# Performance work log

Measured on AMD Instinct MI355X. Metric: run time of the kernel, lower is better.

The kernel has to match this reference:

```python
import jax, jax.numpy as jnp
import numpy as np

B, T, C = 8, 2048, 640

def setup_inputs() -> dict:
    key = jax.random.key(0)
    k1, k2, k3, k4 = jax.random.split(key, 4)
    s = 1.0 / np.sqrt(C)  # ~ torch Linear default init scale
    x = jax.random.normal(k1, (B, T, C), dtype=jnp.float32)
    w_q = jax.random.normal(k2, (C, C), dtype=jnp.float32) * s
    w_k = jax.random.normal(k3, (C, C), dtype=jnp.float32) * s
    w_v = jax.random.normal(k4, (C, C), dtype=jnp.float32) * s
    return {"x": x, "w_q": w_q, "w_k": w_k, "w_v": w_v}

def reference(x, w_q, w_k, w_v):
    # nn.Linear computes x @ W.T; weights here stored as (out, in) like torch.
    q = jnp.einsum('btc,oc->bto', x, w_q)
    k = jnp.einsum('btc,oc->bto', x, w_k)
    v = jnp.einsum('btc,oc->bto', x, w_v)
    scale = jnp.sqrt(jnp.asarray(C, dtype=x.dtype))  # note: full n_embd, not per-head
    scores = jnp.einsum('bqc,bkc->bqk', q, k) / scale  # [B,T,T]
    Tn = x.shape[1]
    causal = jnp.triu(jnp.ones((Tn, Tn), dtype=bool), k=1)
    scores = jnp.where(causal[None, :, :], jnp.asarray(-jnp.inf, dtype=x.dtype), scores)
    attn = jax.nn.softmax(scores, axis=-1)
    attn_out = jnp.einsum('bqk,bkc->bqc', attn, v)
    return x + attn_out
```

## Files before the change

kernel.cpp:

```cpp
#include <hip/hip_runtime.h>
#include <stdint.h>
#include <stddef.h>

#define T_SEQ 2048
#define C_DIM 640
#define N_BATCH 8

typedef __bf16 bf16x8 __attribute__((ext_vector_type(8)));
typedef float f32x4 __attribute__((ext_vector_type(4)));

__device__ __forceinline__ unsigned short f2bf(float f) {
  unsigned u = __float_as_uint(f);
  u += 0x7fffu + ((u >> 16) & 1u);
  return (unsigned short)(u >> 16);
}
__device__ __forceinline__ float bf2f(unsigned short h) {
  return __uint_as_float(((unsigned)h) << 16);
}

__device__ __forceinline__ void gll16(const unsigned short* src, unsigned short* dst) {
  __builtin_amdgcn_global_load_lds(
      (const __attribute__((address_space(1))) void*)src,
      (__attribute__((address_space(3))) void*)dst, 16, 0, 0);
}

__device__ __forceinline__ void stage_tile(const unsigned short* gbase, int ldg,
                                           unsigned short* lbuf, int wave, int lane) {
#pragma unroll
  for (int i = 0; i < 4; ++i) {
    const int o   = i * 4096 + wave * 1024 + lane * 16;
    const int row = o >> 7;
    const int cb  = o & 127;
    const int scb = cb ^ ((row & 7) << 4);
    const unsigned short* src = gbase + (size_t)row * ldg + (scb >> 1);
    unsigned short* dst = lbuf + ((i * 4096 + wave * 1024) >> 1);
    gll16(src, dst);
  }
}

__device__ __forceinline__ void tri_decode(int t, int& mi, int& ni) {
  int m = (int)((__fsqrt_rn(8.0f * (float)t + 1.0f) - 1.0f) * 0.5f);
  while ((m + 1) * (m + 2) / 2 <= t) ++m;
  while (m * (m + 1) / 2 > t) --m;
  mi = m;
  ni = t - m * (m + 1) / 2;
}

template <int MODE>
__global__ __launch_bounds__(256) void gemm_k(
    const unsigned short* __restrict__ Abase, const unsigned short* __restrict__ Bbase,
    const unsigned short* __restrict__ B2base, unsigned short* __restrict__ OutB,
    unsigned short* __restrict__ OutB2, float* __restrict__ OutF,
    const float* __restrict__ Lrow, const unsigned short* __restrict__ Xres,
    float* __restrict__ Lpart) {
  const int lin = blockIdx.x;
  int mi, ni, bz;
  if constexpr (MODE == 0) {
    const int wg = (lin & 7) * 160 + (lin >> 3);
    mi = wg / 10;
    const int t = wg % 10;
    bz = t / 5;
    ni = t % 5;
  } else if constexpr (MODE == 1) {
    const int wg = (lin & 7) * 136 + (lin >> 3);
    bz = wg / 136;
    tri_decode(wg % 136, mi, ni);
  } else if constexpr (MODE == 2) {
    const int wg = (lin & 7) * 80 + (lin >> 3);
    bz = wg / 80;
    const int t = wg % 80;
    mi = 15 - t / 5;
    ni = t % 5;
  } else {
    bz = lin / 25;
    const int rem = lin % 25;
    mi = rem / 5;
    ni = rem % 5;
  }

  __shared__ unsigned short As[2][8192];
  __shared__ unsigned short Bs[2][8192];
  const int tid = threadIdx.x;
  const int wave = tid >> 6, lane = tid & 63;
  const int wm = wave >> 1, wn = wave & 1;

  const unsigned short* Ap;
  const unsigned short* Bp;
  int ldA, ldB, ksteps;
  if constexpr (MODE == 0) {
    Ap = Abase + (size_t)mi * 81920;
    Bp = ((bz == 0) ? Bbase : B2base) + (size_t)ni * 81920;
    ldA = 640; ldB = 640; ksteps = 10;
  } else if constexpr (MODE == 1) {
    Ap = Abase + (size_t)bz * 1310720 + (size_t)mi * 81920;
    Bp = Bbase + (size_t)bz * 1310720 + (size_t)ni * 81920;
    ldA = 640; ldB = 640; ksteps = 10;
  } else if constexpr (MODE == 2) {
    Ap = Abase + (size_t)bz * 4194304 + (size_t)mi * 262144;
    Bp = Bbase + (size_t)bz * 1310720 + (size_t)ni * 262144;
    ldA = 2048; ldB = 2048; ksteps = 2 * (mi + 1);
  } else {
    Ap = Abase + (size_t)mi * 81920 + bz * 128;
    Bp = Bbase + (size_t)ni * 81920 + bz * 128;
    ldA = 640; ldB = 640; ksteps = 2;
  }

  f32x4 acc[4][4] = {};

  stage_tile(Ap, ldA, As[0], wave, lane);
  stage_tile(Bp, ldB, Bs[0], wave, lane);
  __syncthreads();

  int cur = 0;
  for (int t = 0; t < ksteps; ++t) {
    if (t + 1 < ksteps) {
      stage_tile(Ap + (size_t)(t + 1) * 64, ldA, As[cur ^ 1], wave, lane);
      stage_tile(Bp + (size_t)(t + 1) * 64, ldB, Bs[cur ^ 1], wave, lane);
    }
#pragma unroll
    for (int kk = 0; kk < 2; ++kk) {
      bf16x8 af[4], bfr[4];
#pragma unroll
      for (int mt = 0; mt < 4; ++mt) {
        const int row = wm * 64 + mt * 16 + (lane & 15);
        const int cb  = kk * 64 + ((lane >> 4) << 4);
        af[mt] = *(const bf16x8*)&As[cur][row * 64 + ((cb ^ ((row & 7) << 4)) >> 1)];
      }
#pragma unroll
      for (int nt = 0; nt < 4; ++nt) {
        const int row = wn * 64 + nt * 16 + (lane & 15);
        const int cb  = kk * 64 + ((lane >> 4) << 4);
        bfr[nt] = *(const bf16x8*)&Bs[cur][row * 64 + ((cb ^ ((row & 7) << 4)) >> 1)];
      }
#pragma unroll
      for (int mt = 0; mt < 4; ++mt)
#pragma unroll
        for (int nt = 0; nt < 4; ++nt)
          acc[mt][nt] = __builtin_amdgcn_mfma_f32_16x16x32_bf16(af[mt], bfr[nt],
                                                                acc[mt][nt], 0, 0, 0);
    }
    __syncthreads();
    cur ^= 1;
  }

  if constexpr (MODE == 1) {
#pragma unroll
    for (int mt = 0; mt < 4; ++mt) {
      const int r0 = wm * 64 + mt * 16 + ((lane >> 4) << 2);
      const int grow = mi * 128 + r0;
      float rsum[4] = {0.f, 0.f, 0.f, 0.f};
#pragma unroll
      for (int nt = 0; nt < 4; ++nt) {
        const int gc = ni * 128 + wn * 64 + nt * 16 + (lane & 15);
        const size_t base = (size_t)bz * 4194304 + (size_t)grow * 2048 + gc;
#pragma unroll
        for (int r = 0; r < 4; ++r) {
          const float e = (gc <= grow + r) ? __expf(acc[mt][nt][r]) : 0.0f;
          OutB[base + (size_t)r * 2048] = f2bf(e);
          rsum[r] += e;
        }
      }
#pragma unroll
      for (int off = 1; off < 16; off <<= 1) {
#pragma unroll
        for (int r = 0; r < 4; ++r) rsum[r] += __shfl_xor(rsum[r], off);
      }
      if ((lane & 15) == 0) {
#pragma unroll
        for (int r = 0; r < 4; ++r)
          Lpart[((size_t)bz * 2048 + grow + r) * 32 + ni * 2 + wn] = rsum[r];
      }
    }
  } else {
#pragma unroll
    for (int mt = 0; mt < 4; ++mt) {
#pragma unroll
      for (int nt = 0; nt < 4; ++nt) {
        const int r0 = wm * 64 + mt * 16 + ((lane >> 4) << 2);
        const int c  = wn * 64 + nt * 16 + (lane & 15);
        if constexpr (MODE == 0) {
          if (bz == 0) {
            const size_t base = (size_t)(mi * 128 + r0) * 640 + ni * 128 + c;
#pragma unroll
            for (int r = 0; r < 4; ++r) OutB[base + (size_t)r * 640] = f2bf(acc[mt][nt][r]);
          } else {
            const int b = mi >> 4;
            const int tloc = ((mi & 15) << 7) + r0;
            const int gc = ni * 128 + c;
            ushort4 o4;
            o4.x = f2bf(acc[mt][nt][0]); o4.y = f2bf(acc[mt][nt][1]);
            o4.z = f2bf(acc[mt][nt][2]); o4.w = f2bf(acc[mt][nt][3]);
            *(ushort4*)&OutB2[(size_t)b * 1310720 + (size_t)gc * 2048 + tloc] = o4;
          }
        } else if constexpr (MODE == 2) {
          const int grow = mi * 128 + r0;
          const size_t base = (size_t)bz * 1310720 + (size_t)grow * 640 + ni * 128 + c;
#pragma unroll
          for (int r = 0; r < 4; ++r) {
            const float l = Lrow[(size_t)bz * 2048 + grow + r];
            OutF[base + (size_t)r * 640] =
                acc[mt][nt][r] / l + bf2f(Xres[base + (size_t)r * 640]);
          }
        } else {
          const size_t base = (size_t)bz * 409600 + (size_t)(mi * 128 + r0) * 640 + ni * 128 + c;
#pragma unroll
          for (int r = 0; r < 4; ++r) OutF[base + (size_t)r * 640] = acc[mt][nt][r];
        }
      }
    }
  }
}

__global__ void cast_x_k(const float* __restrict__ x, unsigned short* __restrict__ xb, int n4) {
  const int stride = gridDim.x * blockDim.x;
  for (int i = blockIdx.x * blockDim.x + threadIdx.x; i < n4; i += stride) {
    const float4 v = ((const float4*)x)[i];
    ushort4 o;
    o.x = f2bf(v.x); o.y = f2bf(v.y); o.z = f2bf(v.z); o.w = f2bf(v.w);
    ((ushort4*)xb)[i] = o;
  }
}

__global__ void tcast_w(const float* __restrict__ wq, const float* __restrict__ wk,
                        const float* __restrict__ wv, unsigned short* __restrict__ wqT,
                        unsigned short* __restrict__ wkT, unsigned short* __restrict__ wvb) {
  const int z = blockIdx.y;
  const int tx = threadIdx.x, ty = threadIdx.y;
  if (z == 2) {
    const int e = (blockIdx.x * 256 + ty * 32 + tx) * 4;
    const float4 v = *(const float4*)&wv[e];
    ushort4 o;
    o.x = f2bf(v.x); o.y = f2bf(v.y); o.z = f2bf(v.z); o.w = f2bf(v.w);
    *(ushort4*)&wvb[e] = o;
    return;
  }
  __shared__ float tile[32][33];
  const float* w = (z == 0) ? wq : wk;
  unsigned short* wT = (z == 0) ? wqT : wkT;
  const float s = (z == 0) ? 0.03952847075210474f : 1.0f;
  const int bo = (blockIdx.x / 20) * 32, bc = (blockIdx.x % 20) * 32;
#pragma unroll
  for (int i = 0; i < 4; ++i)
    tile[ty + i * 8][tx] = w[(size_t)(bo + ty + i * 8) * 640 + bc + tx];
  __syncthreads();
#pragma unroll
  for (int i = 0; i < 4; ++i)
    wT[(size_t)(bc + ty + i * 8) * 640 + bo + tx] = f2bf(tile[tx][ty + i * 8] * s);
}

__global__ void reduce_mt(const float* __restrict__ Mpart, unsigned short* __restrict__ Mt) {
  const int e = (blockIdx.x * 256 + threadIdx.x) * 4;
  float4 a = *(const float4*)&Mpart[e];
#pragma unroll
  for (int p = 1; p < 5; ++p) {
    const float4 b = *(const float4*)&Mpart[(size_t)p * 409600 + e];
    a.x += b.x; a.y += b.y; a.z += b.z; a.w += b.w;
  }
  ushort4 o;
  o.x = f2bf(a.x); o.y = f2bf(a.y); o.z = f2bf(a.z); o.w = f2bf(a.w);
  *(ushort4*)&Mt[e] = o;
}

__global__ void rowsum_k(const float* __restrict__ Lpart, float* __restrict__ Lr) {
  const int i = blockIdx.x * 256 + threadIdx.x;
  const int jmax = (((i & 2047) >> 7) + 1) * 2;
  const float* p = Lpart + (size_t)i * 32;
  float s = 0.f;
  for (int j = 0; j < jmax; ++j) s += p[j];
  Lr[i] = s;
}

extern "C" void kernel_launch(void* const* d_in, const int* in_sizes, int n_in,
                              void* d_out, int out_size, void* d_ws, size_t ws_size,
                              hipStream_t stream) {
  (void)in_sizes; (void)n_in; (void)out_size; (void)ws_size;
  const float* x  = (const float*)d_in[0];
  const float* wq = (const float*)d_in[1];
  const float* wk = (const float*)d_in[2];
  const float* wv = (const float*)d_in[3];
  float* out = (float*)d_out;

  char* ws = (char*)d_ws;
  unsigned short* xb  = (unsigned short*)(ws + 0);
  unsigned short* wqT = (unsigned short*)(ws + 20971520);
  unsigned short* wkT = (unsigned short*)(ws + 21790720);
  unsigned short* wvb = (unsigned short*)(ws + 22609920);
  unsigned short* Mt  = (unsigned short*)(ws + 23429120);
  unsigned short* y   = (unsigned short*)(ws + 24248320);
  unsigned short* Vt  = (unsigned short*)(ws + 45219840);
  float*          Mpart = (float*)(ws + 66191360);
  float*          Lpart = (float*)(ws + 74383360);
  float*          Lr  = (float*)(ws + 76480512);
  unsigned short* Sb  = (unsigned short*)(ws + 76546048);

  cast_x_k<<<2048, 256, 0, stream>>>(x, xb, 2621440);
  tcast_w<<<dim3(400, 3), dim3(32, 8), 0, stream>>>(wq, wk, wv, wqT, wkT, wvb);
  gemm_k<3><<<125, 256, 0, stream>>>(wkT, wqT, nullptr, nullptr, nullptr, Mpart,
                                     nullptr, nullptr, nullptr);
  reduce_mt<<<400, 256, 0, stream>>>(Mpart, Mt);
  gemm_k<0><<<1280, 256, 0, stream>>>(xb, Mt, wvb, y, Vt, nullptr, nullptr, nullptr,
                                      nullptr);
  gemm_k<1><<<1088, 256, 0, stream>>>(y, xb, nullptr, Sb, nullptr, nullptr, nullptr,
                                      nullptr, Lpart);
  rowsum_k<<<64, 256, 0, stream>>>(Lpart, Lr);
  gemm_k<2><<<640, 256, 0, stream>>>(Sb, Vt, nullptr, nullptr, nullptr, out, Lr, xb,
                                     nullptr);
}
```

Baseline: 152.9 us.

## Fuse score and PV GEMMs into persistent kernel with dependency counters

Replaces the separate score GEMM, row-sum kernel and PV GEMM with one persistent kernel. Workgroups pull work units from an atomic queue ordered by row block, largest first. PV tiles spin-wait on per-(batch,row-block) completion counters and compute the softmax row sums inline. The aim is to remove two kernel launches, the tail idle time between phases, and the separate Lr buffer, at the cost of spin-wait stalls, atomic traffic and possible deadlock if the queue ordering were ever violated.

After: 497.6 us. +225.3%, slower.

```diff
diff --git a/kernel.cpp b/kernel.cpp
--- a/kernel.cpp
+++ b/kernel.cpp
@@ -38,21 +38,11 @@
   }
 }
 
-__device__ __forceinline__ void tri_decode(int t, int& mi, int& ni) {
-  int m = (int)((__fsqrt_rn(8.0f * (float)t + 1.0f) - 1.0f) * 0.5f);
-  while ((m + 1) * (m + 2) / 2 <= t) ++m;
-  while (m * (m + 1) / 2 > t) --m;
-  mi = m;
-  ni = t - m * (m + 1) / 2;
-}
-
 template <int MODE>
 __global__ __launch_bounds__(256) void gemm_k(
     const unsigned short* __restrict__ Abase, const unsigned short* __restrict__ Bbase,
     const unsigned short* __restrict__ B2base, unsigned short* __restrict__ OutB,
-    unsigned short* __restrict__ OutB2, float* __restrict__ OutF,
-    const float* __restrict__ Lrow, const unsigned short* __restrict__ Xres,
-    float* __restrict__ Lpart) {
+    unsigned short* __restrict__ OutB2, float* __restrict__ OutF) {
   const int lin = blockIdx.x;
   int mi, ni, bz;
   if constexpr (MODE == 0) {
@@ -61,16 +51,6 @@
     const int t = wg % 10;
     bz = t / 5;
     ni = t % 5;
-  } else if constexpr (MODE == 1) {
-    const int wg = (lin & 7) * 136 + (lin >> 3);
-    bz = wg / 136;
-    tri_decode(wg % 136, mi, ni);
-  } else if constexpr (MODE == 2) {
-    const int wg = (lin & 7) * 80 + (lin >> 3);
-    bz = wg / 80;
-    const int t = wg % 80;
-    mi = 15 - t / 5;
-    ni = t % 5;
   } else {
     bz = lin / 25;
     const int rem = lin % 25;
@@ -86,36 +66,27 @@
 
   const unsigned short* Ap;
   const unsigned short* Bp;
-  int ldA, ldB, ksteps;
+  int ksteps;
   if constexpr (MODE == 0) {
     Ap = Abase + (size_t)mi * 81920;
     Bp = ((bz == 0) ? Bbase : B2base) + (size_t)ni * 81920;
-    ldA = 640; ldB = 640; ksteps = 10;
-  } else if constexpr (MODE == 1) {
-    Ap = Abase + (size_t)bz * 1310720 + (size_t)mi * 81920;
-    Bp = Bbase + (size_t)bz * 1310720 + (size_t)ni * 81920;
-    ldA = 640; ldB = 640; ksteps = 10;
-  } else if constexpr (MODE == 2) {
-    Ap = Abase + (size_t)bz * 4194304 + (size_t)mi * 262144;
-    Bp = Bbase + (size_t)bz * 1310720 + (size_t)ni * 262144;
-    ldA = 2048; ldB = 2048; ksteps = 2 * (mi + 1);
+    ksteps = 10;
   } else {
     Ap = Abase + (size_t)mi * 81920 + bz * 128;
     Bp = Bbase + (size_t)ni * 81920 + bz * 128;
-    ldA = 640; ldB = 640; ksteps = 2;
+    ksteps = 2;
   }
 
   f32x4 acc[4][4] = {};
-
-  stage_tile(Ap, ldA, As[0], wave, lane);
-  stage_tile(Bp, ldB, Bs[0], wave, lane);
+  stage_tile(Ap, 640, As[0], wave, lane);
+  stage_tile(Bp, 640, Bs[0], wave, lane);
   __syncthreads();
 
   int cur = 0;
   for (int t = 0; t < ksteps; ++t) {
     if (t + 1 < ksteps) {
-      stage_tile(Ap + (size_t)(t + 1) * 64, ldA, As[cur ^ 1], wave, lane);
-      stage_tile(Bp + (size_t)(t + 1) * 64, ldB, Bs[cur ^ 1], wave, lane);
+      stage_tile(Ap + (size_t)(t + 1) * 64, 640, As[cur ^ 1], wave, lane);
+      stage_tile(Bp + (size_t)(t + 1) * 64, 640, Bs[cur ^ 1], wave, lane);
     }
 #pragma unroll
     for (int kk = 0; kk < 2; ++kk) {
@@ -143,68 +114,176 @@
     cur ^= 1;
   }
 
-  if constexpr (MODE == 1) {
-#pragma unroll
-    for (int mt = 0; mt < 4; ++mt) {
+#pragma unroll
+  for (int mt = 0; mt < 4; ++mt) {
+#pragma unroll
+    for (int nt = 0; nt < 4; ++nt) {
       const int r0 = wm * 64 + mt * 16 + ((lane >> 4) << 2);
-      const int grow = mi * 128 + r0;
-      float rsum[4] = {0.f, 0.f, 0.f, 0.f};
-#pragma unroll
-      for (int nt = 0; nt < 4; ++nt) {
-        const int gc = ni * 128 + wn * 64 + nt * 16 + (lane & 15);
-        const size_t base = (size_t)bz * 4194304 + (size_t)grow * 2048 + gc;
-#pragma unroll
-        for (int r = 0; r < 4; ++r) {
-          const float e = (gc <= grow + r) ? __expf(acc[mt][nt][r]) : 0.0f;
-          OutB[base + (size_t)r * 2048] = f2bf(e);
-          rsum[r] += e;
-        }
-      }
-#pragma unroll
-      for (int off = 1; off < 16; off <<= 1) {
-#pragma unroll
-        for (int r = 0; r < 4; ++r) rsum[r] += __shfl_xor(rsum[r], off);
-      }
-      if ((lane & 15) == 0) {
-#pragma unroll
-        for (int r = 0; r < 4; ++r)
-          Lpart[((size_t)bz * 2048 + grow + r) * 32 + ni * 2 + wn] = rsum[r];
-      }
-    }
-  } else {
-#pragma unroll
-    for (int mt = 0; mt < 4; ++mt) {
-#pragma unroll
-      for (int nt = 0; nt < 4; ++nt) {
+      const int c  = wn * 64 + nt * 16 + (lane & 15);
+      if constexpr (MODE == 0) {
+        if (bz == 0) {
+          const size_t base = (size_t)(mi * 128 + r0) * 640 + ni * 128 + c;
+#pragma unroll
+          for (int r = 0; r < 4; ++r) OutB[base + (size_t)r * 640] = f2bf(acc[mt][nt][r]);
+        } else {
+          const int b = mi >> 4;
+          const int tloc = ((mi & 15) << 7) + r0;
+          const int gc = ni * 128 + c;
+          ushort4 o4;
+          o4.x = f2bf(acc[mt][nt][0]); o4.y = f2bf(acc[mt][nt][1]);
+          o4.z = f2bf(acc[mt][nt][2]); o4.w = f2bf(acc[mt][nt][3]);
+          *(ushort4*)&OutB2[(size_t)b * 1310720 + (size_t)gc * 2048 + tloc] = o4;
+        }
+      } else {
+        const size_t base = (size_t)bz * 409600 + (size_t)(mi * 128 + r0) * 640 + ni * 128 + c;
+#pragma unroll
+        for (int r = 0; r < 4; ++r) OutF[base + (size_t)r * 640] = acc[mt][nt][r];
+      }
+    }
+  }
+}
+
+#define NU 1728
+__global__ __launch_bounds__(256) void attn_k(
+    const unsigned short* __restrict__ y, const unsigned short* __restrict__ xb,
+    const unsigned short* __restrict__ Vt, unsigned short* __restrict__ P,
+    float* __restrict__ Lpart, float* __restrict__ out,
+    int* __restrict__ qctr, int* __restrict__ done) {
+  __shared__ unsigned short As[2][8192];
+  __shared__ unsigned short Bs[2][8192];
+  __shared__ float Ls[128];
+  __shared__ int s_u;
+  const int tid = threadIdx.x;
+  const int wave = tid >> 6, lane = tid & 63;
+  const int wm = wave >> 1, wn = wave & 1;
+
+  for (;;) {
+    __syncthreads();
+    if (tid == 0) s_u = atomicAdd(qctr, 1);
+    __syncthreads();
+    const int u = s_u;
+    if (u >= NU) break;
+
+    int rem = u, mi = 0, sub = 0;
+    bool isPV = false;
+    for (int m = 15; m >= 0; --m) {
+      const int a = 8 * (m + 1);
+      if (rem < a) { mi = m; sub = rem; isPV = false; break; }
+      rem -= a;
+      if (rem < 40) { mi = m; sub = rem; isPV = true; break; }
+      rem -= 40;
+    }
+
+    const unsigned short *Ap, *Bp;
+    int ldA, ldB, ksteps, b, nc;
+    if (!isPV) {
+      b = sub / (mi + 1); nc = sub % (mi + 1);
+      Ap = y  + (size_t)b * 1310720 + (size_t)mi * 81920;
+      Bp = xb + (size_t)b * 1310720 + (size_t)nc * 81920;
+      ldA = 640; ldB = 640; ksteps = 10;
+    } else {
+      b = sub / 5; nc = sub % 5;
+      if (tid == 0) {
+        while (__hip_atomic_load(&done[b * 16 + mi], __ATOMIC_ACQUIRE,
+                                 __HIP_MEMORY_SCOPE_AGENT) < mi + 1)
+          __builtin_amdgcn_s_sleep(1);
+      }
+      __syncthreads();
+      if (tid < 128) {
+        const float* p = &Lpart[((size_t)b * 2048 + mi * 128 + tid) * 32];
+        float s = 0.f;
+        const int jm = 2 * (mi + 1);
+        for (int j = 0; j < jm; ++j) s += p[j];
+        Ls[tid] = 1.0f / s;
+      }
+      Ap = P  + (size_t)b * 4194304 + (size_t)mi * 262144;
+      Bp = Vt + (size_t)b * 1310720 + (size_t)nc * 262144;
+      ldA = 2048; ldB = 2048; ksteps = 2 * (mi + 1);
+    }
+
+    f32x4 acc[4][4] = {};
+    stage_tile(Ap, ldA, As[0], wave, lane);
+    stage_tile(Bp, ldB, Bs[0], wave, lane);
+    __syncthreads();
+
+    int cur = 0;
+    for (int t = 0; t < ksteps; ++t) {
+      if (t + 1 < ksteps) {
+        stage_tile(Ap + (size_t)(t + 1) * 64, ldA, As[cur ^ 1], wave, lane);
+        stage_tile(Bp + (size_t)(t + 1) * 64, ldB, Bs[cur ^ 1], wave, lane);
+      }
+#pragma unroll
+      for (int kk = 0; kk < 2; ++kk) {
+        bf16x8 af[4], bfr[4];
+#pragma unroll
+        for (int mt = 0; mt < 4; ++mt) {
+          const int row = wm * 64 + mt * 16 + (lane & 15);
+          const int cb  = kk * 64 + ((lane >> 4) << 4);
+          af[mt] = *(const bf16x8*)&As[cur][row * 64 + ((cb ^ ((row & 7) << 4)) >> 1)];
+        }
+#pragma unroll
+        for (int nt = 0; nt < 4; ++nt) {
+          const int row = wn * 64 + nt * 16 + (lane & 15);
+          const int cb  = kk * 64 + ((lane >> 4) << 4);
+          bfr[nt] = *(const bf16x8*)&Bs[cur][row * 64 + ((cb ^ ((row & 7) << 4)) >> 1)];
+        }
+#pragma unroll
+        for (int mt = 0; mt < 4; ++mt)
+#pragma unroll
+          for (int nt = 0; nt < 4; ++nt)
+            acc[mt][nt] = __builtin_amdgcn_mfma_f32_16x16x32_bf16(af[mt], bfr[nt],
+                                                                  acc[mt][nt], 0, 0, 0);
+      }
+      __syncthreads();
+      cur ^= 1;
+    }
+
+    if (!isPV) {
+#pragma unroll
+      for (int mt = 0; mt < 4; ++mt) {
         const int r0 = wm * 64 + mt * 16 + ((lane >> 4) << 2);
-        const int c  = wn * 64 + nt * 16 + (lane & 15);
-        if constexpr (MODE == 0) {
-          if (bz == 0) {
-            const size_t base = (size_t)(mi * 128 + r0) * 640 + ni * 128 + c;
-#pragma unroll
-            for (int r = 0; r < 4; ++r) OutB[base + (size_t)r * 640] = f2bf(acc[mt][nt][r]);
-          } else {
-            const int b = mi >> 4;
-            const int tloc = ((mi & 15) << 7) + r0;
-            const int gc = ni * 128 + c;
-            ushort4 o4;
-            o4.x = f2bf(acc[mt][nt][0]); o4.y = f2bf(acc[mt][nt][1]);
-            o4.z = f2bf(acc[mt][nt][2]); o4.w = f2bf(acc[mt][nt][3]);
-            *(ushort4*)&OutB2[(size_t)b * 1310720 + (size_t)gc * 2048 + tloc] = o4;
+        const int grow = mi * 128 + r0;
+        float rsum[4] = {0.f, 0.f, 0.f, 0.f};
+#pragma unroll
+        for (int nt = 0; nt < 4; ++nt) {
+          const int gc = nc * 128 + wn * 64 + nt * 16 + (lane & 15);
+          const size_t base = (size_t)b * 4194304 + (size_t)grow * 2048 + gc;
+#pragma unroll
+          for (int r = 0; r < 4; ++r) {
+            const float e = (gc <= grow + r) ? __expf(acc[mt][nt][r]) : 0.0f;
+            P[base + (size_t)r * 2048] = f2bf(e);
+            rsum[r] += e;
           }
-        } else if constexpr (MODE == 2) {
+        }
+#pragma unroll
+        for (int off = 1; off < 16; off <<= 1) {
+#pragma unroll
+          for (int r = 0; r < 4; ++r) rsum[r] += __shfl_xor(rsum[r], off);
+        }
+        if ((lane & 15) == 0) {
+#pragma unroll
+          for (int r = 0; r < 4; ++r)
+            Lpart[((size_t)b * 2048 + grow + r) * 32 + nc * 2 + wn] = rsum[r];
+        }
+      }
+      __threadfence();
+      __syncthreads();
+      if (tid == 0) atomicAdd(&done[b * 16 + mi], 1);
+    } else {
+#pragma unroll
+      for (int mt = 0; mt < 4; ++mt) {
+#pragma unroll
+        for (int nt = 0; nt < 4; ++nt) {
+          const int r0 = wm * 64 + mt * 16 + ((lane >> 4) << 2);
+          const int c  = wn * 64 + nt * 16 + (lane & 15);
           const int grow = mi * 128 + r0;
-          const size_t base = (size_t)bz * 1310720 + (size_t)grow * 640 + ni * 128 + c;
+          const size_t base = (size_t)b * 1310720 + (size_t)grow * 640 + nc * 128 + c;
 #pragma unroll
           for (int r = 0; r < 4; ++r) {
-            const float l = Lrow[(size_t)bz * 2048 + grow + r];
-            OutF[base + (size_t)r * 640] =
-                acc[mt][nt][r] / l + bf2f(Xres[base + (size_t)r * 640]);
+            const float rl = Ls[r0 + r];
+            out[base + (size_t)r * 640] =
+                acc[mt][nt][r] * rl + bf2f(xb[base + (size_t)r * 640]);
           }
-        } else {
-          const size_t base = (size_t)bz * 409600 + (size_t)(mi * 128 + r0) * 640 + ni * 128 + c;
-#pragma unroll
-          for (int r = 0; r < 4; ++r) OutF[base + (size_t)r * 640] = acc[mt][nt][r];
         }
       }
     }
@@ -261,15 +340,6 @@
   *(ushort4*)&Mt[e] = o;
 }
 
-__global__ void rowsum_k(const float* __restrict__ Lpart, float* __restrict__ Lr) {
-  const int i = blockIdx.x * 256 + threadIdx.x;
-  const int jmax = (((i & 2047) >> 7) + 1) * 2;
-  const float* p = Lpart + (size_t)i * 32;
-  float s = 0.f;
-  for (int j = 0; j < jmax; ++j) s += p[j];
-  Lr[i] = s;
-}
-
 extern "C" void kernel_launch(void* const* d_in, const int* in_sizes, int n_in,
                               void* d_out, int out_size, void* d_ws, size_t ws_size,
                               hipStream_t stream) {
@@ -290,19 +360,14 @@
   unsigned short* Vt  = (unsigned short*)(ws + 45219840);
   float*          Mpart = (float*)(ws + 66191360);
   float*          Lpart = (float*)(ws + 74383360);
-  float*          Lr  = (float*)(ws + 76480512);
   unsigned short* Sb  = (unsigned short*)(ws + 76546048);
-
+  int*            ctrs = (int*)(ws + 143654912);
+
+  hipMemsetAsync(ctrs, 0, 1024, stream);
   cast_x_k<<<2048, 256, 0, stream>>>(x, xb, 2621440);
   tcast_w<<<dim3(400, 3), dim3(32, 8), 0, stream>>>(wq, wk, wv, wqT, wkT, wvb);
-  gemm_k<3><<<125, 256, 0, stream>>>(wkT, wqT, nullptr, nullptr, nullptr, Mpart,
-                                     nullptr, nullptr, nullptr);
+  gemm_k<3><<<125, 256, 0, stream>>>(wkT, wqT, nullptr, nullptr, nullptr, Mpart);
   reduce_mt<<<400, 256, 0, stream>>>(Mpart, Mt);
-  gemm_k<0><<<1280, 256, 0, stream>>>(xb, Mt, wvb, y, Vt, nullptr, nullptr, nullptr,
-                                      nullptr);
-  gemm_k<1><<<1088, 256, 0, stream>>>(y, xb, nullptr, Sb, nullptr, nullptr, nullptr,
-                                      nullptr, Lpart);
-  rowsum_k<<<64, 256, 0, stream>>>(Lpart, Lr);
-  gemm_k<2><<<640, 256, 0, stream>>>(Sb, Vt, nullptr, nullptr, nullptr, out, Lr, xb,
-                                     nullptr);
-}
+  gemm_k<0><<<1280, 256, 0, stream>>>(xb, Mt, wvb, y, Vt, nullptr);
+  attn_k<<<512, 256, 0, stream>>>(y, xb, Vt, Sb, Lpart, out, ctrs, ctrs + 1);
+}
```

## Halve GEMM K-tile to 32 and fold row-sum reduction into output GEMM

Applied to the files above, without the earlier changes.

The per-stage K depth in all GEMM modes drops from 64 to 32 with a new swizzle, so each k-step stages half the LDS and the step count doubles. The aim is a smaller LDS footprint and higher occupancy, at the cost of twice as many barriers and less MFMA work per barrier. The separate rowsum kernel is also removed: the PV GEMM now sums the softmax partials for its 128 rows into shared memory and multiplies by the reciprocal instead of dividing. This saves one launch and a global round trip.

Result: no change. 155.8 us (+1.8%).

```diff
diff --git a/kernel.cpp b/kernel.cpp
--- a/kernel.cpp
+++ b/kernel.cpp
@@ -24,17 +24,16 @@
       (__attribute__((address_space(3))) void*)dst, 16, 0, 0);
 }
 
-__device__ __forceinline__ void stage_tile(const unsigned short* gbase, int ldg,
-                                           unsigned short* lbuf, int wave, int lane) {
-#pragma unroll
-  for (int i = 0; i < 4; ++i) {
-    const int o   = i * 4096 + wave * 1024 + lane * 16;
-    const int row = o >> 7;
-    const int cb  = o & 127;
-    const int scb = cb ^ ((row & 7) << 4);
-    const unsigned short* src = gbase + (size_t)row * ldg + (scb >> 1);
-    unsigned short* dst = lbuf + ((i * 4096 + wave * 1024) >> 1);
-    gll16(src, dst);
+__device__ __forceinline__ void stage_tile32(const unsigned short* gbase, int ldg,
+                                             unsigned short* lbuf, int wave, int lane) {
+#pragma unroll
+  for (int i = 0; i < 2; ++i) {
+    const int o = i * 4096 + wave * 1024 + lane * 16;
+    const int a = o ^ (((o >> 7) & 7) << 4);
+    const int row = a >> 6;
+    const int colb = a & 63;
+    gll16(gbase + (size_t)row * ldg + (colb >> 1),
+          lbuf + ((i * 4096 + wave * 1024) >> 1));
   }
 }
 
@@ -51,8 +50,7 @@
     const unsigned short* __restrict__ Abase, const unsigned short* __restrict__ Bbase,
     const unsigned short* __restrict__ B2base, unsigned short* __restrict__ OutB,
     unsigned short* __restrict__ OutB2, float* __restrict__ OutF,
-    const float* __restrict__ Lrow, const unsigned short* __restrict__ Xres,
-    float* __restrict__ Lpart) {
+    const unsigned short* __restrict__ Xres, float* __restrict__ Lpart) {
   const int lin = blockIdx.x;
   int mi, ni, bz;
   if constexpr (MODE == 0) {
@@ -78,8 +76,8 @@
     ni = rem % 5;
   }
 
-  __shared__ unsigned short As[2][8192];
-  __shared__ unsigned short Bs[2][8192];
+  __shared__ unsigned short As[2][4096];
+  __shared__ unsigned short Bs[2][4096];
   const int tid = threadIdx.x;
   const int wave = tid >> 6, lane = tid & 63;
   const int wm = wave >> 1, wn = wave & 1;
@@ -90,55 +88,62 @@
   if constexpr (MODE == 0) {
     Ap = Abase + (size_t)mi * 81920;
     Bp = ((bz == 0) ? Bbase : B2base) + (size_t)ni * 81920;
-    ldA = 640; ldB = 640; ksteps = 10;
+    ldA = 640; ldB = 640; ksteps = 20;
   } else if constexpr (MODE == 1) {
     Ap = Abase + (size_t)bz * 1310720 + (size_t)mi * 81920;
     Bp = Bbase + (size_t)bz * 1310720 + (size_t)ni * 81920;
-    ldA = 640; ldB = 640; ksteps = 10;
+    ldA = 640; ldB = 640; ksteps = 20;
   } else if constexpr (MODE == 2) {
     Ap = Abase + (size_t)bz * 4194304 + (size_t)mi * 262144;
     Bp = Bbase + (size_t)bz * 1310720 + (size_t)ni * 262144;
-    ldA = 2048; ldB = 2048; ksteps = 2 * (mi + 1);
+    ldA = 2048; ldB = 2048; ksteps = 4 * (mi + 1);
   } else {
     Ap = Abase + (size_t)mi * 81920 + bz * 128;
     Bp = Bbase + (size_t)ni * 81920 + bz * 128;
-    ldA = 640; ldB = 640; ksteps = 2;
+    ldA = 640; ldB = 640; ksteps = 4;
+  }
+
+  __shared__ float Ls[(MODE == 2) ? 128 : 1];
+  if constexpr (MODE == 2) {
+    if (tid < 128) {
+      const float* p = &Lpart[((size_t)bz * 2048 + mi * 128 + tid) * 32];
+      float s = 0.f;
+      const int jm = 2 * (mi + 1);
+      for (int j = 0; j < jm; ++j) s += p[j];
+      Ls[tid] = 1.0f / s;
+    }
   }
 
   f32x4 acc[4][4] = {};
-
-  stage_tile(Ap, ldA, As[0], wave, lane);
-  stage_tile(Bp, ldB, Bs[0], wave, lane);
+  stage_tile32(Ap, ldA, As[0], wave, lane);
+  stage_tile32(Bp, ldB, Bs[0], wave, lane);
   __syncthreads();
 
   int cur = 0;
   for (int t = 0; t < ksteps; ++t) {
     if (t + 1 < ksteps) {
-      stage_tile(Ap + (size_t)(t + 1) * 64, ldA, As[cur ^ 1], wave, lane);
-      stage_tile(Bp + (size_t)(t + 1) * 64, ldB, Bs[cur ^ 1], wave, lane);
-    }
-#pragma unroll
-    for (int kk = 0; kk < 2; ++kk) {
-      bf16x8 af[4], bfr[4];
-#pragma unroll
-      for (int mt = 0; mt < 4; ++mt) {
-        const int row = wm * 64 + mt * 16 + (lane & 15);
-        const int cb  = kk * 64 + ((lane >> 4) << 4);
-        af[mt] = *(const bf16x8*)&As[cur][row * 64 + ((cb ^ ((row & 7) << 4)) >> 1)];
-      }
-#pragma unroll
-      for (int nt = 0; nt < 4; ++nt) {
-        const int row = wn * 64 + nt * 16 + (lane & 15);
-        const int cb  = kk * 64 + ((lane >> 4) << 4);
-        bfr[nt] = *(const bf16x8*)&Bs[cur][row * 64 + ((cb ^ ((row & 7) << 4)) >> 1)];
-      }
-#pragma unroll
-      for (int mt = 0; mt < 4; ++mt)
-#pragma unroll
-        for (int nt = 0; nt < 4; ++nt)
-          acc[mt][nt] = __builtin_amdgcn_mfma_f32_16x16x32_bf16(af[mt], bfr[nt],
-                                                                acc[mt][nt], 0, 0, 0);
-    }
+      stage_tile32(Ap + (size_t)(t + 1) * 32, ldA, As[cur ^ 1], wave, lane);
+      stage_tile32(Bp + (size_t)(t + 1) * 32, ldB, Bs[cur ^ 1], wave, lane);
+    }
+    bf16x8 af[4], bfr[4];
+#pragma unroll
+    for (int mt = 0; mt < 4; ++mt) {
+      const int r = wm * 64 + mt * 16 + (lane & 15);
+      const int a = r * 64 + ((lane >> 4) << 4);
+      af[mt] = *(const bf16x8*)&As[cur][(a ^ (((a >> 7) & 7) << 4)) >> 1];
+    }
+#pragma unroll
+    for (int nt = 0; nt < 4; ++nt) {
+      const int r = wn * 64 + nt * 16 + (lane & 15);
+      const int a = r * 64 + ((lane >> 4) << 4);
+      bfr[nt] = *(const bf16x8*)&Bs[cur][(a ^ (((a >> 7) & 7) << 4)) >> 1];
+    }
+#pragma unroll
+    for (int mt = 0; mt < 4; ++mt)
+#pragma unroll
+      for (int nt = 0; nt < 4; ++nt)
+        acc[mt][nt] = __builtin_amdgcn_mfma_f32_16x16x32_bf16(af[mt], bfr[nt],
+                                                              acc[mt][nt], 0, 0, 0);
     __syncthreads();
     cur ^= 1;
   }
@@ -197,9 +202,8 @@
           const size_t base = (size_t)bz * 1310720 + (size_t)grow * 640 + ni * 128 + c;
 #pragma unroll
           for (int r = 0; r < 4; ++r) {
-            const float l = Lrow[(size_t)bz * 2048 + grow + r];
             OutF[base + (size_t)r * 640] =
-                acc[mt][nt][r] / l + bf2f(Xres[base + (size_t)r * 640]);
+                acc[mt][nt][r] * Ls[r0 + r] + bf2f(Xres[base + (size_t)r * 640]);
           }
         } else {
           const size_t base = (size_t)bz * 409600 + (size_t)(mi * 128 + r0) * 640 + ni * 128 + c;
@@ -261,15 +265,6 @@
   *(ushort4*)&Mt[e] = o;
 }
 
-__global__ void rowsum_k(const float* __restrict__ Lpart, float* __restrict__ Lr) {
-  const int i = blockIdx.x * 256 + threadIdx.x;
-  const int jmax = (((i & 2047) >> 7) + 1) * 2;
-  const float* p = Lpart + (size_t)i * 32;
-  float s = 0.f;
-  for (int j = 0; j < jmax; ++j) s += p[j];
-  Lr[i] = s;
-}
-
 extern "C" void kernel_launch(void* const* d_in, const int* in_sizes, int n_in,
                               void* d_out, int out_size, void* d_ws, size_t ws_size,
                               hipStream_t stream) {
@@ -290,19 +285,16 @@
   unsigned short* Vt  = (unsigned short*)(ws + 45219840);
   float*          Mpart = (float*)(ws + 66191360);
   float*          Lpart = (float*)(ws + 74383360);
-  float*          Lr  = (float*)(ws + 76480512);
   unsigned short* Sb  = (unsigned short*)(ws + 76546048);
 
   cast_x_k<<<2048, 256, 0, stream>>>(x, xb, 2621440);
   tcast_w<<<dim3(400, 3), dim3(32, 8), 0, stream>>>(wq, wk, wv, wqT, wkT, wvb);
   gemm_k<3><<<125, 256, 0, stream>>>(wkT, wqT, nullptr, nullptr, nullptr, Mpart,
-                                     nullptr, nullptr, nullptr);
+                                     nullptr, nullptr);
   reduce_mt<<<400, 256, 0, stream>>>(Mpart, Mt);
-  gemm_k<0><<<1280, 256, 0, stream>>>(xb, Mt, wvb, y, Vt, nullptr, nullptr, nullptr,
-                                      nullptr);
+  gemm_k<0><<<1280, 256, 0, stream>>>(xb, Mt, wvb, y, Vt, nullptr, nullptr, nullptr);
   gemm_k<1><<<1088, 256, 0, stream>>>(y, xb, nullptr, Sb, nullptr, nullptr, nullptr,
-                                      nullptr, Lpart);
-  rowsum_k<<<64, 256, 0, stream>>>(Lpart, Lr);
-  gemm_k<2><<<640, 256, 0, stream>>>(Sb, Vt, nullptr, nullptr, nullptr, out, Lr, xb,
-                                     nullptr);
-}
+                                      Lpart);
+  gemm_k<2><<<640, 256, 0, stream>>>(Sb, Vt, nullptr, nullptr, nullptr, out, xb,
+                                     Lpart);
+}
```
